# Optimization experiments

Measured on AMD Instinct MI355X. Metric: run time of the kernel, lower is better.

Reference implementation:

```python
import jax, jax.numpy as jnp
import numpy as np

HIDDEN = 2048
N_HEADS = 16
N_KV_HEADS = 4
HEAD_DIM = HIDDEN // N_HEADS  # 128
WINDOW = 2048
ROPE_THETA = 10000.0


def setup_inputs() -> dict:
    key = jax.random.key(0)
    ks = jax.random.split(key, 5)
    B, S = 1, 4096
    scale = 0.02
    return {
        "hidden_states": jax.random.normal(ks[0], (B, S, HIDDEN), dtype=jnp.float32),
        # nn.Linear weights are [out_features, in_features]
        "q_w": jax.random.normal(ks[1], (N_HEADS * HEAD_DIM, HIDDEN), dtype=jnp.float32) * scale,
        "k_w": jax.random.normal(ks[2], (N_KV_HEADS * HEAD_DIM, HIDDEN), dtype=jnp.float32) * scale,
        "v_w": jax.random.normal(ks[3], (N_KV_HEADS * HEAD_DIM, HIDDEN), dtype=jnp.float32) * scale,
        "o_w": jax.random.normal(ks[4], (HIDDEN, N_HEADS * HEAD_DIM), dtype=jnp.float32) * scale,
    }


def _rope_cos_sin(seq_len, dtype):
    inv_freq = 1.0 / (ROPE_THETA ** (jnp.arange(0, HEAD_DIM, 2, dtype=jnp.float32) / HEAD_DIM))
    pos = jnp.arange(seq_len, dtype=jnp.float32)
    freqs = pos[:, None] * inv_freq[None, :]          # [S, D/2]
    emb = jnp.concatenate([freqs, freqs], axis=-1)    # [S, D]
    return jnp.cos(emb).astype(dtype), jnp.sin(emb).astype(dtype)


def _rotate_half(x):
    x1, x2 = jnp.split(x, 2, axis=-1)
    return jnp.concatenate([-x2, x1], axis=-1)


def reference(hidden_states, q_w, k_w, v_w, o_w):
    B, S, _ = hidden_states.shape
    dtype = hidden_states.dtype

    q = hidden_states @ q_w.T                         # [B,S,H*D]
    k = hidden_states @ k_w.T                         # [B,S,Hkv*D]
    v = hidden_states @ v_w.T

    q = q.reshape(B, S, N_HEADS, HEAD_DIM).transpose(0, 2, 1, 3)      # [B,H,S,D]
    k = k.reshape(B, S, N_KV_HEADS, HEAD_DIM).transpose(0, 2, 1, 3)   # [B,Hkv,S,D]
    v = v.reshape(B, S, N_KV_HEADS, HEAD_DIM).transpose(0, 2, 1, 3)

    cos, sin = _rope_cos_sin(S, dtype)                # [S,D]
    cos = cos[None, None]
    sin = sin[None, None]
    q = q * cos + _rotate_half(q) * sin
    k = k * cos + _rotate_half(k) * sin

    n_rep = N_HEADS // N_KV_HEADS
    k = jnp.repeat(k, n_rep, axis=1)                  # [B,H,S,D]
    v = jnp.repeat(v, n_rep, axis=1)

    scores = jnp.einsum("bhqd,bhkd->bhqk", q, k) / jnp.sqrt(jnp.array(HEAD_DIM, dtype))

    pos = jnp.arange(S)
    rel = pos[:, None] - pos[None, :]
    allowed = (rel >= 0) & (rel < WINDOW)             # causal sliding window
    mask = jnp.where(allowed, jnp.array(0.0, dtype), jnp.array(-jnp.inf, dtype))
    scores = scores + mask[None, None]

    attn = jax.nn.softmax(scores.astype(jnp.float32), axis=-1).astype(dtype)

    out = jnp.einsum("bhqk,bhkd->bhqd", attn, v)      # [B,H,S,D]
    out = out.transpose(0, 2, 1, 3).reshape(B, S, N_HEADS * HEAD_DIM)
    return out @ o_w.T
```

## Files before the change

kernel.cpp:

```cpp
#include <hip/hip_runtime.h>
#include <stdint.h>

typedef unsigned short u16;
typedef unsigned int u32;
typedef float f32x4 __attribute__((ext_vector_type(4)));
typedef float f32x8 __attribute__((ext_vector_type(8)));
typedef int   i32x4 __attribute__((ext_vector_type(4)));
typedef __bf16 bf16x8 __attribute__((ext_vector_type(8)));
typedef u16 u16x4 __attribute__((ext_vector_type(4)));

constexpr int S_LEN = 4096;
constexpr int HID   = 2048;
constexpr int WIN   = 2048;

__device__ __forceinline__ u32 f2bf_u(float f) {
  u32 u = __builtin_bit_cast(u32, f);
  return (u + 0x7fffu + ((u >> 16) & 1u)) >> 16;
}
__device__ __forceinline__ float bf2f(u16 u) {
  return __builtin_bit_cast(float, ((u32)u) << 16);
}
__device__ __forceinline__ float exp2x(float x) {
#if __has_builtin(__builtin_amdgcn_exp2f)
  return __builtin_amdgcn_exp2f(x);
#else
  return exp2f(x);
#endif
}
__device__ __forceinline__ void mfma16(f32x4& acc, i32x4 a, i32x4 b) {
  acc = __builtin_amdgcn_mfma_f32_16x16x32_bf16(
      __builtin_bit_cast(bf16x8, a), __builtin_bit_cast(bf16x8, b), acc, 0, 0, 0);
}
__device__ __forceinline__ void gload_lds16(const u16* g, u16* l) {
  __builtin_amdgcn_global_load_lds((const __attribute__((address_space(1))) u32*)g,
                                   (__attribute__((address_space(3))) u32*)l, 16, 0, 0);
}

constexpr int CVT_B0 = 1048576;
constexpr int CVT_B1 = CVT_B0 + 524288;
constexpr int CVT_B2 = CVT_B1 + 131072;
constexpr int CVT_B3 = CVT_B2 + 131072;
constexpr int CVT_B4 = CVT_B3 + 524288;

__global__ __launch_bounds__(256) void cvt_all_kernel(
    const float* __restrict__ s0, const float* __restrict__ s1,
    const float* __restrict__ s2, const float* __restrict__ s3,
    const float* __restrict__ s4, u16* __restrict__ d0, u16* __restrict__ d1,
    u16* __restrict__ d2, u16* __restrict__ d3, u16* __restrict__ d4) {
  int t = blockIdx.x * 256 + threadIdx.x;
  const float* s;
  u16* d;
  int off;
  if (t < CVT_B0) { s = s0; d = d0; off = t; }
  else if (t < CVT_B1) { s = s1; d = d1; off = t - CVT_B0; }
  else if (t < CVT_B2) { s = s2; d = d2; off = t - CVT_B1; }
  else if (t < CVT_B3) { s = s3; d = d3; off = t - CVT_B2; }
  else { s = s4; d = d4; off = t - CVT_B3; }
  const f32x4* sp = (const f32x4*)s + (size_t)off * 2;
  f32x4 a = sp[0], b = sp[1];
  i32x4 o;
  o.x = (int)(f2bf_u(a.x) | (f2bf_u(a.y) << 16));
  o.y = (int)(f2bf_u(a.z) | (f2bf_u(a.w) << 16));
  o.z = (int)(f2bf_u(b.x) | (f2bf_u(b.y) << 16));
  o.w = (int)(f2bf_u(b.z) | (f2bf_u(b.w) << 16));
  *((i32x4*)d + off) = o;
}

__global__ __launch_bounds__(256) void rope_table_kernel(float* __restrict__ cs,
                                                         float* __restrict__ sn) {
  int t = blockIdx.x * 256 + threadIdx.x;
  int d = t & 63, s = t >> 6;
  float inv = exp2f(-(float)d * 0.20762050593046014f);
  float f = (float)s * inv;
  cs[t] = cosf(f);
  sn[t] = sinf(f);
}

__global__ __launch_bounds__(256) void rope_qk_kernel(u16* __restrict__ Qb,
                                                      u16* __restrict__ Kb,
                                                      const float* __restrict__ cs,
                                                      const float* __restrict__ sn) {
  const float SC2 = 0.088388347648318447f * 1.4426950408889634f;
  int t = blockIdx.x * 256 + threadIdx.x;
  int d0 = (t & 15) * 4;
  int r = t >> 4;
  u16* p;
  int s;
  float qs;
  if (r < S_LEN * 16) {
    int h = r & 15; s = r >> 4;
    p = Qb + (size_t)s * HID + h * 128 + d0;
    qs = SC2;
  } else {
    int r2 = r - S_LEN * 16;
    int h = r2 & 3; s = r2 >> 2;
    p = Kb + (size_t)s * 512 + h * 128 + d0;
    qs = 1.f;
  }
  f32x4 c = *(const f32x4*)&cs[(s << 6) | d0];
  f32x4 si = *(const f32x4*)&sn[(s << 6) | d0];
  u16x4 a = *(u16x4*)p, b = *(u16x4*)(p + 64);
  u16x4 oa, ob;
#pragma unroll
  for (int j = 0; j < 4; ++j) {
    float x1 = bf2f(a[j]), x2 = bf2f(b[j]);
    oa[j] = (u16)f2bf_u((x1 * c[j] - x2 * si[j]) * qs);
    ob[j] = (u16)f2bf_u((x2 * c[j] + x1 * si[j]) * qs);
  }
  *(u16x4*)p = oa;
  *(u16x4*)(p + 64) = ob;
}

__global__ __launch_bounds__(256) void qkv_gemm_kernel(
    const u16* __restrict__ A, const u16* __restrict__ Wq,
    const u16* __restrict__ Wk, const u16* __restrict__ Wv,
    u16* __restrict__ Qb, u16* __restrict__ Kb, u16* __restrict__ Vt) {
  __shared__ __attribute__((aligned(16))) u16 sA[128 * 64];
  __shared__ __attribute__((aligned(16))) u16 sB[128 * 64];
  const int lane = threadIdx.x & 63;
  const int w = threadIdx.x >> 6;
  const int g = lane >> 4, ln = lane & 15;
  const int K = HID;

  int wgid = blockIdx.x;
  wgid = (wgid & 7) * 96 + (wgid >> 3);
  const int brow = (wgid / 24) * 128;
  const int bcol = (wgid % 24) * 128;

  const u16* B;
  u16* out;
  int bc, mode, N;
  if (bcol < 2048)      { B = Wq; out = Qb; bc = bcol;        N = 2048; mode = 0; }
  else if (bcol < 2560) { B = Wk; out = Kb; bc = bcol - 2048; N = 512;  mode = 0; }
  else                  { B = Wv; out = Vt; bc = bcol - 2560; N = 512;  mode = 1; }

  const int wr = (w >> 1) * 64, wc = (w & 1) * 64;
  f32x4 acc[4][4] = {};

  const int sr = w * 32 + (lane >> 3);
  const int scol = (lane & 7) * 8;
  const u16* Abase = A + (size_t)(brow + sr) * K + scol;
  const u16* Bbase = B + (size_t)(bc + sr) * K + scol;
  u16* sAdst = &sA[w * 2048];
  u16* sBdst = &sB[w * 2048];

  for (int k0 = 0; k0 < K; k0 += 64) {
    __syncthreads();
#pragma unroll
    for (int i = 0; i < 4; ++i) {
      gload_lds16(Abase + (size_t)i * 8 * K + k0, sAdst + i * 512);
      gload_lds16(Bbase + (size_t)i * 8 * K + k0, sBdst + i * 512);
    }
    __syncthreads();
#pragma unroll
    for (int kk = 0; kk < 2; ++kk) {
      i32x4 af[4], bfr[4];
#pragma unroll
      for (int m = 0; m < 4; ++m)
        af[m] = *(const i32x4*)&sA[(wr + m * 16 + ln) * 64 + kk * 32 + g * 8];
#pragma unroll
      for (int n = 0; n < 4; ++n)
        bfr[n] = *(const i32x4*)&sB[(wc + n * 16 + ln) * 64 + kk * 32 + g * 8];
#pragma unroll
      for (int m = 0; m < 4; ++m)
#pragma unroll
        for (int n = 0; n < 4; ++n) mfma16(acc[m][n], af[m], bfr[n]);
    }
  }

  const int orow0 = brow + wr + g * 4;
  const int ocol0 = bc + wc + ln;
#pragma unroll
  for (int m = 0; m < 4; ++m)
#pragma unroll
    for (int n = 0; n < 4; ++n)
#pragma unroll
      for (int j = 0; j < 4; ++j) {
        int row = orow0 + m * 16 + j;
        int col = ocol0 + n * 16;
        float v = acc[m][n][j];
        if (mode == 0) {
          out[(size_t)row * N + col] = (u16)f2bf_u(v);
        } else {
          int d = col & 127, kvh = col >> 7;
          int T = row >> 5, ks = row & 31;
          int tt = ks >> 4, gg = (ks >> 2) & 3, e = (tt << 2) | (ks & 3);
          size_t idx = (size_t)kvh * S_LEN * 128 + (size_t)T * 4096 +
                       (size_t)d * 32 + ((size_t)(gg ^ ((d >> 1) & 3)) << 3) + e;
          out[idx] = (u16)f2bf_u(v);
        }
      }
}

__global__ __launch_bounds__(256) void gemm_o_kernel(const u16* __restrict__ A,
                                                     const u16* __restrict__ B,
                                                     float* __restrict__ Cv,
                                                     int K, int N) {
  __shared__ __attribute__((aligned(16))) u16 sA[128 * 64];
  __shared__ __attribute__((aligned(16))) u16 sB[128 * 64];
  const int lane = threadIdx.x & 63;
  const int w = threadIdx.x >> 6;
  const int g = lane >> 4, ln = lane & 15;

  int wgid = blockIdx.y * gridDim.x + blockIdx.x;
  const int nwg = gridDim.x * gridDim.y;
  wgid = (wgid & 7) * (nwg >> 3) + (wgid >> 3);
  const int brow = (wgid / gridDim.x) * 128;
  const int bcol = (wgid % gridDim.x) * 128;
  const int wr = (w >> 1) * 64, wc = (w & 1) * 64;

  f32x4 acc[4][4] = {};

  const int sr = w * 32 + (lane >> 3);
  const int scol = (lane & 7) * 8;
  const u16* Abase = A + (size_t)(brow + sr) * K + scol;
  const u16* Bbase = B + (size_t)(bcol + sr) * K + scol;
  u16* sAdst = &sA[w * 2048];
  u16* sBdst = &sB[w * 2048];

  for (int k0 = 0; k0 < K; k0 += 64) {
    __syncthreads();
#pragma unroll
    for (int i = 0; i < 4; ++i) {
      gload_lds16(Abase + (size_t)i * 8 * K + k0, sAdst + i * 512);
      gload_lds16(Bbase + (size_t)i * 8 * K + k0, sBdst + i * 512);
    }
    __syncthreads();
#pragma unroll
    for (int kk = 0; kk < 2; ++kk) {
      i32x4 af[4], bfr[4];
#pragma unroll
      for (int m = 0; m < 4; ++m)
        af[m] = *(const i32x4*)&sA[(wr + m * 16 + ln) * 64 + kk * 32 + g * 8];
#pragma unroll
      for (int n = 0; n < 4; ++n)
        bfr[n] = *(const i32x4*)&sB[(wc + n * 16 + ln) * 64 + kk * 32 + g * 8];
#pragma unroll
      for (int m = 0; m < 4; ++m)
#pragma unroll
        for (int n = 0; n < 4; ++n) mfma16(acc[m][n], af[m], bfr[n]);
    }
  }

  const int orow0 = brow + wr + g * 4;
  const int ocol0 = bcol + wc + ln;
#pragma unroll
  for (int m = 0; m < 4; ++m)
#pragma unroll
    for (int n = 0; n < 4; ++n)
#pragma unroll
      for (int j = 0; j < 4; ++j)
        Cv[(size_t)(orow0 + m * 16 + j) * N + ocol0 + n * 16] = acc[m][n][j];
}

__global__ __launch_bounds__(64) void attn_kernel(const u16* __restrict__ Q,
                                                  const u16* __restrict__ Kb,
                                                  const u16* __restrict__ Vt,
                                                  u16* __restrict__ opart,
                                                  float* __restrict__ mpart,
                                                  float* __restrict__ lpart) {
  const int lane = threadIdx.x;
  const int g = lane >> 4, ln = lane & 15;

  const int o = blockIdx.x;
  const int wgid = ((o & 7) << 9) | (o >> 3);
  const int h = wgid >> 8;
  const int idx = wgid & 255;
  const int chunk = idx & 1;
  const int gq = 127 - (idx >> 1);
  const int kvh = h >> 2;
  const int qr0 = gq * 32;

  i32x4 aq[2][4];
#pragma unroll
  for (int qf = 0; qf < 2; ++qf) {
    const u16* qp = Q + (size_t)(qr0 + qf * 16 + ln) * HID + h * 128 + g * 8;
#pragma unroll
    for (int c = 0; c < 4; ++c) aq[qf][c] = *(const i32x4*)(qp + c * 32);
  }

  f32x4 oacc[2][8] = {};
  float mrun[2] = {-1e30f, -1e30f};
  float lrun[2] = {0.f, 0.f};

  int lo = qr0 - (WIN - 1);
  if (lo < 0) lo = 0;
  lo &= ~31;
  const int nt_full = ((qr0 + 32) - lo) >> 5;
  const int nt0 = nt_full >> 1;
  const int lo_c = lo + (chunk ? nt0 * 32 : 0);
  const int nt = chunk ? nt_full - nt0 : nt0;

  const u16* kptr = Kb + (size_t)(lo_c + ln) * 512 + kvh * 128 + g * 8;
  const int vswz = (g ^ ((ln >> 1) & 3)) << 3;
  const u16* vptr = Vt + (size_t)kvh * S_LEN * 128 +
                    (size_t)(lo_c >> 5) * 4096 + ln * 32 + vswz;

  i32x4 kf[2][4], vf[8];
  if (nt > 0) {
#pragma unroll
    for (int t = 0; t < 2; ++t)
#pragma unroll
      for (int c = 0; c < 4; ++c)
        kf[t][c] = *(const i32x4*)(kptr + t * 8192 + c * 32);
#pragma unroll
    for (int nf = 0; nf < 8; ++nf) vf[nf] = *(const i32x4*)(vptr + nf * 512);
  }

  for (int it = 0; it < nt; ++it) {
    const int kb = lo_c + it * 32;
    const bool more = (it + 1 < nt);

    f32x4 sc[2][2] = {};
    __builtin_amdgcn_s_setprio(1);
#pragma unroll
    for (int c = 0; c < 4; ++c) {
      mfma16(sc[0][0], kf[0][c], aq[0][c]);
      mfma16(sc[0][1], kf[1][c], aq[0][c]);
      mfma16(sc[1][0], kf[0][c], aq[1][c]);
      mfma16(sc[1][1], kf[1][c], aq[1][c]);
    }
    __builtin_amdgcn_s_setprio(0);

    if (more) {
      kptr += 32 * 512;
#pragma unroll
      for (int t = 0; t < 2; ++t)
#pragma unroll
        for (int c = 0; c < 4; ++c)
          kf[t][c] = *(const i32x4*)(kptr + t * 8192 + c * 32);
    }

    float p[2][8];
    float mx[2];
    const bool interior = (kb + 31 <= qr0) && (qr0 + 31 - kb < WIN);
#pragma unroll
    for (int qf = 0; qf < 2; ++qf) {
      if (interior) {
#pragma unroll
        for (int j = 0; j < 4; ++j) {
          p[qf][j] = sc[qf][0][j];
          p[qf][4 + j] = sc[qf][1][j];
        }
      } else {
        const float NEG = -__builtin_inff();
        const int q = qr0 + qf * 16 + ln;
#pragma unroll
        for (int t = 0; t < 2; ++t)
#pragma unroll
          for (int j = 0; j < 4; ++j) {
            int k = kb + t * 16 + g * 4 + j;
            p[qf][t * 4 + j] = (k <= q && q - k < WIN) ? sc[qf][t][j] : NEG;
          }
      }
      float x0 = fmaxf(fmaxf(p[qf][0], p[qf][1]), p[qf][2]);
      float x1 = fmaxf(fmaxf(p[qf][3], p[qf][4]), p[qf][5]);
      float x2 = fmaxf(fmaxf(p[qf][6], p[qf][7]), x0);
      float m = fmaxf(x1, x2);
      m = fmaxf(m, __shfl_xor(m, 16));
      m = fmaxf(m, __shfl_xor(m, 32));
      mx[qf] = m;
    }

    float corr[2] = {1.f, 1.f};
    const bool noskip =
        !__all((mx[0] - mrun[0] <= 11.f) && (mx[1] - mrun[1] <= 11.f));
    if (noskip) {
#pragma unroll
      for (int qf = 0; qf < 2; ++qf) {
        float mnew = fmaxf(mrun[qf], mx[qf]);
        corr[qf] = exp2x(mrun[qf] - mnew);
        mrun[qf] = mnew;
        f32x4 cv;
#pragma unroll
        for (int j = 0; j < 4; ++j) cv[j] = __shfl(corr[qf], g * 4 + j);
#pragma unroll
        for (int nf = 0; nf < 8; ++nf)
#pragma unroll
          for (int j = 0; j < 4; ++j) oacc[qf][nf][j] *= cv[j];
      }
    }

    i32x4 pa[2];
#pragma unroll
    for (int qf = 0; qf < 2; ++qf) {
      f32x8 pv;
#pragma unroll
      for (int e = 0; e < 8; ++e) pv[e] = exp2x(p[qf][e] - mrun[qf]);
      float rs = ((pv[0] + pv[1]) + (pv[2] + pv[3])) +
                 ((pv[4] + pv[5]) + (pv[6] + pv[7]));
      lrun[qf] = lrun[qf] * corr[qf] + rs;
      bf16x8 pb = __builtin_convertvector(pv, bf16x8);
      pa[qf] = __builtin_bit_cast(i32x4, pb);
    }

    __builtin_amdgcn_s_setprio(1);
#pragma unroll
    for (int nf = 0; nf < 8; ++nf) {
      mfma16(oacc[0][nf], pa[0], vf[nf]);
      mfma16(oacc[1][nf], pa[1], vf[nf]);
    }
    __builtin_amdgcn_s_setprio(0);

    if (more) {
      vptr += 4096;
#pragma unroll
      for (int nf = 0; nf < 8; ++nf) vf[nf] = *(const i32x4*)(vptr + nf * 512);
    }
  }

#pragma unroll
  for (int qf = 0; qf < 2; ++qf) {
    float l = lrun[qf];
    l += __shfl_xor(l, 16);
    l += __shfl_xor(l, 32);
    lrun[qf] = l;
  }

  const size_t pb = ((size_t)chunk * 16 + h) * S_LEN;
#pragma unroll
  for (int qf = 0; qf < 2; ++qf) {
    if (g == 0) {
      mpart[pb + qr0 + qf * 16 + ln] = mrun[qf];
      lpart[pb + qr0 + qf * 16 + ln] = lrun[qf];
    }
    u16* aop = opart + (pb + qr0 + qf * 16 + g * 4) * 128 + ln;
#pragma unroll
    for (int j = 0; j < 4; ++j)
#pragma unroll
      for (int nf = 0; nf < 8; ++nf)
        aop[(size_t)j * 128 + nf * 16] = (u16)f2bf_u(oacc[qf][nf][j]);
  }
}

__global__ __launch_bounds__(256) void attn_combine_kernel(
    const u16* __restrict__ opart, const float* __restrict__ mpart,
    const float* __restrict__ lpart, u16* __restrict__ AO) {
  int t = blockIdx.x * 256 + threadIdx.x;
  int d0 = (t & 15) * 8;
  int rh = t >> 4;
  int row = rh & (S_LEN - 1);
  int h = rh >> 12;
  size_t i0 = (size_t)h * S_LEN + row;
  size_t i1 = i0 + (size_t)16 * S_LEN;
  float m0 = mpart[i0], m1 = mpart[i1];
  float l0 = lpart[i0], l1 = lpart[i1];
  float m = fmaxf(m0, m1);
  float w0 = exp2x(m0 - m), w1 = exp2x(m1 - m);
  float inv = 1.f / (l0 * w0 + l1 * w1);
  w0 *= inv;
  w1 *= inv;
  i32x4 v0 = *(const i32x4*)(opart + i0 * 128 + d0);
  i32x4 v1 = *(const i32x4*)(opart + i1 * 128 + d0);
  i32x4 ov;
#pragma unroll
  for (int j = 0; j < 4; ++j) {
    u32 a = ((u32)v0[j]), b = ((u32)v1[j]);
    float x = bf2f((u16)a) * w0 + bf2f((u16)b) * w1;
    float y = bf2f((u16)(a >> 16)) * w0 + bf2f((u16)(b >> 16)) * w1;
    ov[j] = (int)(f2bf_u(x) | (f2bf_u(y) << 16));
  }
  *(i32x4*)(AO + (size_t)row * HID + h * 128 + d0) = ov;
}

extern "C" void kernel_launch(void* const* d_in, const int* in_sizes, int n_in,
                              void* d_out, int out_size, void* d_ws, size_t ws_size,
                              hipStream_t stream) {
  const float* hx = (const float*)d_in[0];
  const float* qw = (const float*)d_in[1];
  const float* kw = (const float*)d_in[2];
  const float* vw = (const float*)d_in[3];
  const float* ow = (const float*)d_in[4];

  char* p = (char*)d_ws;
  u16* Xb = (u16*)p; p += (size_t)S_LEN * HID * 2;
  u16* Wq = (u16*)p; p += (size_t)HID * HID * 2;
  u16* Wk = (u16*)p; p += (size_t)512 * HID * 2;
  u16* Wv = (u16*)p; p += (size_t)512 * HID * 2;
  u16* Wo = (u16*)p; p += (size_t)HID * HID * 2;
  u16* Qb = (u16*)p; p += (size_t)S_LEN * HID * 2;
  u16* Kb = (u16*)p; p += (size_t)S_LEN * 512 * 2;
  u16* Vt = (u16*)p; p += (size_t)S_LEN * 512 * 2;
  u16* AO = (u16*)p; p += (size_t)S_LEN * HID * 2;
  float* cs = (float*)p; p += (size_t)S_LEN * 64 * 4;
  float* sn = (float*)p; p += (size_t)S_LEN * 64 * 4;
  u16* Opart = (u16*)p; p += (size_t)2 * 16 * S_LEN * 128 * 2;
  float* Mpart = (float*)p; p += (size_t)2 * 16 * S_LEN * 4;
  float* Lpart = (float*)p; p += (size_t)2 * 16 * S_LEN * 4;

  cvt_all_kernel<<<CVT_B4 / 256, 256, 0, stream>>>(hx, qw, kw, vw, ow, Xb, Wq,
                                                   Wk, Wv, Wo);
  rope_table_kernel<<<S_LEN * 64 / 256, 256, 0, stream>>>(cs, sn);

  qkv_gemm_kernel<<<768, 256, 0, stream>>>(Xb, Wq, Wk, Wv, Qb, Kb, Vt);

  rope_qk_kernel<<<S_LEN * 20 * 16 / 256, 256, 0, stream>>>(Qb, Kb, cs, sn);

  attn_kernel<<<4096, 64, 0, stream>>>(Qb, Kb, Vt, Opart, Mpart, Lpart);
  attn_combine_kernel<<<S_LEN * 16 * 16 / 256, 256, 0, stream>>>(Opart, Mpart,
                                                                 Lpart, AO);

  gemm_o_kernel<<<dim3(16, 32), 256, 0, stream>>>(AO, Wo, (float*)d_out, HID,
                                                  HID);
}
```

Measured before the change: 315.6 us.

## Double-buffer swizzled 256x128 GEMM core for QKV and O projections; fold rope table into convert

Replaces the two single-buffered 128x128 GEMMs with a shared 256x128-tile core run by 512-thread blocks. The core double-buffers LDS via global_load_lds with vmcnt waits and XOR-swizzles the LDS layout to cut bank conflicts. It also folds rope table generation into the conversion kernel, removing one launch. This raises LDS use to 96KB per block, which limits occupancy, and reduces grid sizes to 384 and 256 blocks.

Result: faster. 298.0 us (median of 3 runs) (-5.6%).

```diff
diff --git a/kernel.cpp b/kernel.cpp
--- a/kernel.cpp
+++ b/kernel.cpp
@@ -41,13 +41,28 @@
 constexpr int CVT_B2 = CVT_B1 + 131072;
 constexpr int CVT_B3 = CVT_B2 + 131072;
 constexpr int CVT_B4 = CVT_B3 + 524288;
+constexpr int CVT_B5 = CVT_B4 + 32768;
 
 __global__ __launch_bounds__(256) void cvt_all_kernel(
     const float* __restrict__ s0, const float* __restrict__ s1,
     const float* __restrict__ s2, const float* __restrict__ s3,
     const float* __restrict__ s4, u16* __restrict__ d0, u16* __restrict__ d1,
-    u16* __restrict__ d2, u16* __restrict__ d3, u16* __restrict__ d4) {
+    u16* __restrict__ d2, u16* __restrict__ d3, u16* __restrict__ d4,
+    float* __restrict__ cs, float* __restrict__ sn) {
   int t = blockIdx.x * 256 + threadIdx.x;
+  if (t >= CVT_B4) {
+    if (t >= CVT_B5) return;
+    int e = (t - CVT_B4) * 8;
+    int d = e & 63, s = e >> 6;
+#pragma unroll
+    for (int j = 0; j < 8; ++j) {
+      float inv = exp2f(-(float)(d + j) * 0.20762050593046014f);
+      float f = (float)s * inv;
+      cs[e + j] = cosf(f);
+      sn[e + j] = sinf(f);
+    }
+    return;
+  }
   const float* s;
   u16* d;
   int off;
@@ -64,16 +79,6 @@
   o.z = (int)(f2bf_u(b.x) | (f2bf_u(b.y) << 16));
   o.w = (int)(f2bf_u(b.z) | (f2bf_u(b.w) << 16));
   *((i32x4*)d + off) = o;
-}
-
-__global__ __launch_bounds__(256) void rope_table_kernel(float* __restrict__ cs,
-                                                         float* __restrict__ sn) {
-  int t = blockIdx.x * 256 + threadIdx.x;
-  int d = t & 63, s = t >> 6;
-  float inv = exp2f(-(float)d * 0.20762050593046014f);
-  float f = (float)s * inv;
-  cs[t] = cosf(f);
-  sn[t] = sinf(f);
 }
 
 __global__ __launch_bounds__(256) void rope_qk_kernel(u16* __restrict__ Qb,
@@ -111,65 +116,96 @@
   *(u16x4*)(p + 64) = ob;
 }
 
-__global__ __launch_bounds__(256) void qkv_gemm_kernel(
+__device__ __forceinline__ void gemm256_core(const u16* __restrict__ A_,
+                                             const u16* __restrict__ Bm_,
+                                             int brow_, int bc_,
+                                             f32x4 (&acc)[4][4], int& orow0,
+                                             int& ocol0) {
+  __shared__ __attribute__((aligned(16))) u16 sA[2][256 * 64];
+  __shared__ __attribute__((aligned(16))) u16 sB[2][128 * 64];
+  const int t = threadIdx.x;
+  const int lane = t & 63;
+  const int w = t >> 6;
+  const int g = lane >> 4, ln = lane & 15;
+  const int wm = w >> 1, wn = w & 1;
+  const int trow = t >> 3, tslot = t & 7;
+  const int sslot = tslot ^ (trow & 7);
+  const u16* Abase = A_ + (size_t)(brow_ + trow) * 2048 + sslot * 8;
+  const u16* Bbase = Bm_ + (size_t)(bc_ + trow) * 2048 + sslot * 8;
+
+#define STAGE6(buf, kt)                                                        \
+  {                                                                            \
+    const int _k0 = (kt) * 64;                                                 \
+    _Pragma("unroll") for (int a2 = 0; a2 < 4; ++a2)                           \
+        gload_lds16(Abase + (size_t)a2 * 64 * 2048 + _k0,                      \
+                    &sA[buf][a2 * 4096 + t * 8]);                              \
+    _Pragma("unroll") for (int b2 = 0; b2 < 2; ++b2)                           \
+        gload_lds16(Bbase + (size_t)b2 * 64 * 2048 + _k0,                      \
+                    &sB[buf][b2 * 4096 + t * 8]);                              \
+  }
+
+  STAGE6(0, 0);
+  STAGE6(1, 1);
+  asm volatile("s_waitcnt vmcnt(6)" ::: "memory");
+  __builtin_amdgcn_s_barrier();
+  int cur = 0;
+  for (int kt = 0; kt < 32; ++kt) {
+    i32x4 bfr[4][2];
+#pragma unroll
+    for (int n = 0; n < 4; ++n) {
+      const int row = wn * 64 + n * 16 + ln;
+      const int sw = row & 7;
+      bfr[n][0] = *(const i32x4*)&sB[cur][row * 64 + ((g ^ sw) << 3)];
+      bfr[n][1] = *(const i32x4*)&sB[cur][row * 64 + (((4 | g) ^ sw) << 3)];
+    }
+    __builtin_amdgcn_s_setprio(1);
+#pragma unroll
+    for (int m = 0; m < 4; ++m) {
+      const int row = wm * 64 + m * 16 + ln;
+      const int sw = row & 7;
+      i32x4 a0 = *(const i32x4*)&sA[cur][row * 64 + ((g ^ sw) << 3)];
+      i32x4 a1 = *(const i32x4*)&sA[cur][row * 64 + (((4 | g) ^ sw) << 3)];
+#pragma unroll
+      for (int n = 0; n < 4; ++n) {
+        mfma16(acc[m][n], a0, bfr[n][0]);
+        mfma16(acc[m][n], a1, bfr[n][1]);
+      }
+    }
+    __builtin_amdgcn_s_setprio(0);
+    __builtin_amdgcn_s_barrier();
+    if (kt + 2 < 32) {
+      STAGE6(cur, kt + 2);
+      asm volatile("s_waitcnt vmcnt(6)" ::: "memory");
+    } else if (kt + 1 < 32) {
+      asm volatile("s_waitcnt vmcnt(0)" ::: "memory");
+    }
+    __builtin_amdgcn_s_barrier();
+    cur ^= 1;
+  }
+#undef STAGE6
+  orow0 = brow_ + wm * 64 + g * 4;
+  ocol0 = bc_ + wn * 64 + ln;
+}
+
+__global__ __launch_bounds__(512) void qkv256_kernel(
     const u16* __restrict__ A, const u16* __restrict__ Wq,
     const u16* __restrict__ Wk, const u16* __restrict__ Wv,
     u16* __restrict__ Qb, u16* __restrict__ Kb, u16* __restrict__ Vt) {
-  __shared__ __attribute__((aligned(16))) u16 sA[128 * 64];
-  __shared__ __attribute__((aligned(16))) u16 sB[128 * 64];
-  const int lane = threadIdx.x & 63;
-  const int w = threadIdx.x >> 6;
-  const int g = lane >> 4, ln = lane & 15;
-  const int K = HID;
-
   int wgid = blockIdx.x;
-  wgid = (wgid & 7) * 96 + (wgid >> 3);
-  const int brow = (wgid / 24) * 128;
+  wgid = (wgid & 7) * 48 + (wgid >> 3);
+  const int brow = (wgid / 24) * 256;
   const int bcol = (wgid % 24) * 128;
-
-  const u16* B;
+  const u16* Bm;
   u16* out;
   int bc, mode, N;
-  if (bcol < 2048)      { B = Wq; out = Qb; bc = bcol;        N = 2048; mode = 0; }
-  else if (bcol < 2560) { B = Wk; out = Kb; bc = bcol - 2048; N = 512;  mode = 0; }
-  else                  { B = Wv; out = Vt; bc = bcol - 2560; N = 512;  mode = 1; }
-
-  const int wr = (w >> 1) * 64, wc = (w & 1) * 64;
+  if (bcol < 2048)      { Bm = Wq; out = Qb; bc = bcol;        N = 2048; mode = 0; }
+  else if (bcol < 2560) { Bm = Wk; out = Kb; bc = bcol - 2048; N = 512;  mode = 0; }
+  else                  { Bm = Wv; out = Vt; bc = bcol - 2560; N = 512;  mode = 1; }
+
   f32x4 acc[4][4] = {};
-
-  const int sr = w * 32 + (lane >> 3);
-  const int scol = (lane & 7) * 8;
-  const u16* Abase = A + (size_t)(brow + sr) * K + scol;
-  const u16* Bbase = B + (size_t)(bc + sr) * K + scol;
-  u16* sAdst = &sA[w * 2048];
-  u16* sBdst = &sB[w * 2048];
-
-  for (int k0 = 0; k0 < K; k0 += 64) {
-    __syncthreads();
-#pragma unroll
-    for (int i = 0; i < 4; ++i) {
-      gload_lds16(Abase + (size_t)i * 8 * K + k0, sAdst + i * 512);
-      gload_lds16(Bbase + (size_t)i * 8 * K + k0, sBdst + i * 512);
-    }
-    __syncthreads();
-#pragma unroll
-    for (int kk = 0; kk < 2; ++kk) {
-      i32x4 af[4], bfr[4];
-#pragma unroll
-      for (int m = 0; m < 4; ++m)
-        af[m] = *(const i32x4*)&sA[(wr + m * 16 + ln) * 64 + kk * 32 + g * 8];
-#pragma unroll
-      for (int n = 0; n < 4; ++n)
-        bfr[n] = *(const i32x4*)&sB[(wc + n * 16 + ln) * 64 + kk * 32 + g * 8];
-#pragma unroll
-      for (int m = 0; m < 4; ++m)
-#pragma unroll
-        for (int n = 0; n < 4; ++n) mfma16(acc[m][n], af[m], bfr[n]);
-    }
-  }
-
-  const int orow0 = brow + wr + g * 4;
-  const int ocol0 = bc + wc + ln;
+  int orow0, ocol0;
+  gemm256_core(A, Bm, brow, bc, acc, orow0, ocol0);
+
 #pragma unroll
   for (int m = 0; m < 4; ++m)
 #pragma unroll
@@ -192,65 +228,25 @@
       }
 }
 
-__global__ __launch_bounds__(256) void gemm_o_kernel(const u16* __restrict__ A,
-                                                     const u16* __restrict__ B,
-                                                     float* __restrict__ Cv,
-                                                     int K, int N) {
-  __shared__ __attribute__((aligned(16))) u16 sA[128 * 64];
-  __shared__ __attribute__((aligned(16))) u16 sB[128 * 64];
-  const int lane = threadIdx.x & 63;
-  const int w = threadIdx.x >> 6;
-  const int g = lane >> 4, ln = lane & 15;
-
-  int wgid = blockIdx.y * gridDim.x + blockIdx.x;
-  const int nwg = gridDim.x * gridDim.y;
-  wgid = (wgid & 7) * (nwg >> 3) + (wgid >> 3);
-  const int brow = (wgid / gridDim.x) * 128;
-  const int bcol = (wgid % gridDim.x) * 128;
-  const int wr = (w >> 1) * 64, wc = (w & 1) * 64;
+__global__ __launch_bounds__(512) void o256_kernel(const u16* __restrict__ A,
+                                                   const u16* __restrict__ Bw,
+                                                   float* __restrict__ Cv) {
+  int wgid = blockIdx.x;
+  wgid = (wgid & 7) * 32 + (wgid >> 3);
+  const int brow = (wgid / 16) * 256;
+  const int bcol = (wgid % 16) * 128;
 
   f32x4 acc[4][4] = {};
-
-  const int sr = w * 32 + (lane >> 3);
-  const int scol = (lane & 7) * 8;
-  const u16* Abase = A + (size_t)(brow + sr) * K + scol;
-  const u16* Bbase = B + (size_t)(bcol + sr) * K + scol;
-  u16* sAdst = &sA[w * 2048];
-  u16* sBdst = &sB[w * 2048];
-
-  for (int k0 = 0; k0 < K; k0 += 64) {
-    __syncthreads();
-#pragma unroll
-    for (int i = 0; i < 4; ++i) {
-      gload_lds16(Abase + (size_t)i * 8 * K + k0, sAdst + i * 512);
-      gload_lds16(Bbase + (size_t)i * 8 * K + k0, sBdst + i * 512);
-    }
-    __syncthreads();
-#pragma unroll
-    for (int kk = 0; kk < 2; ++kk) {
-      i32x4 af[4], bfr[4];
-#pragma unroll
-      for (int m = 0; m < 4; ++m)
-        af[m] = *(const i32x4*)&sA[(wr + m * 16 + ln) * 64 + kk * 32 + g * 8];
-#pragma unroll
-      for (int n = 0; n < 4; ++n)
-        bfr[n] = *(const i32x4*)&sB[(wc + n * 16 + ln) * 64 + kk * 32 + g * 8];
-#pragma unroll
-      for (int m = 0; m < 4; ++m)
-#pragma unroll
-        for (int n = 0; n < 4; ++n) mfma16(acc[m][n], af[m], bfr[n]);
-    }
-  }
-
-  const int orow0 = brow + wr + g * 4;
-  const int ocol0 = bcol + wc + ln;
+  int orow0, ocol0;
+  gemm256_core(A, Bw, brow, bcol, acc, orow0, ocol0);
+
 #pragma unroll
   for (int m = 0; m < 4; ++m)
 #pragma unroll
     for (int n = 0; n < 4; ++n)
 #pragma unroll
       for (int j = 0; j < 4; ++j)
-        Cv[(size_t)(orow0 + m * 16 + j) * N + ocol0 + n * 16] = acc[m][n][j];
+        Cv[(size_t)(orow0 + m * 16 + j) * 2048 + ocol0 + n * 16] = acc[m][n][j];
 }
 
 __global__ __launch_bounds__(64) void attn_kernel(const u16* __restrict__ Q,
@@ -299,10 +295,10 @@
   i32x4 kf[2][4], vf[8];
   if (nt > 0) {
 #pragma unroll
-    for (int t = 0; t < 2; ++t)
+    for (int tt = 0; tt < 2; ++tt)
 #pragma unroll
       for (int c = 0; c < 4; ++c)
-        kf[t][c] = *(const i32x4*)(kptr + t * 8192 + c * 32);
+        kf[tt][c] = *(const i32x4*)(kptr + tt * 8192 + c * 32);
 #pragma unroll
     for (int nf = 0; nf < 8; ++nf) vf[nf] = *(const i32x4*)(vptr + nf * 512);
   }
@@ -325,10 +321,10 @@
     if (more) {
       kptr += 32 * 512;
 #pragma unroll
-      for (int t = 0; t < 2; ++t)
+      for (int tt = 0; tt < 2; ++tt)
 #pragma unroll
         for (int c = 0; c < 4; ++c)
-          kf[t][c] = *(const i32x4*)(kptr + t * 8192 + c * 32);
+          kf[tt][c] = *(const i32x4*)(kptr + tt * 8192 + c * 32);
     }
 
     float p[2][8];
@@ -346,11 +342,11 @@
         const float NEG = -__builtin_inff();
         const int q = qr0 + qf * 16 + ln;
 #pragma unroll
-        for (int t = 0; t < 2; ++t)
+        for (int tt = 0; tt < 2; ++tt)
 #pragma unroll
           for (int j = 0; j < 4; ++j) {
-            int k = kb + t * 16 + g * 4 + j;
-            p[qf][t * 4 + j] = (k <= q && q - k < WIN) ? sc[qf][t][j] : NEG;
+            int k = kb + tt * 16 + g * 4 + j;
+            p[qf][tt * 4 + j] = (k <= q && q - k < WIN) ? sc[qf][tt][j] : NEG;
           }
       }
       float x0 = fmaxf(fmaxf(p[qf][0], p[qf][1]), p[qf][2]);
@@ -488,11 +484,10 @@
   float* Mpart = (float*)p; p += (size_t)2 * 16 * S_LEN * 4;
   float* Lpart = (float*)p; p += (size_t)2 * 16 * S_LEN * 4;
 
-  cvt_all_kernel<<<CVT_B4 / 256, 256, 0, stream>>>(hx, qw, kw, vw, ow, Xb, Wq,
-                                                   Wk, Wv, Wo);
-  rope_table_kernel<<<S_LEN * 64 / 256, 256, 0, stream>>>(cs, sn);
-
-  qkv_gemm_kernel<<<768, 256, 0, stream>>>(Xb, Wq, Wk, Wv, Qb, Kb, Vt);
+  cvt_all_kernel<<<(CVT_B5 + 255) / 256, 256, 0, stream>>>(
+      hx, qw, kw, vw, ow, Xb, Wq, Wk, Wv, Wo, cs, sn);
+
+  qkv256_kernel<<<384, 512, 0, stream>>>(Xb, Wq, Wk, Wv, Qb, Kb, Vt);
 
   rope_qk_kernel<<<S_LEN * 20 * 16 / 256, 256, 0, stream>>>(Qb, Kb, cs, sn);
 
@@ -500,6 +495,5 @@
   attn_combine_kernel<<<S_LEN * 16 * 16 / 256, 256, 0, stream>>>(Opart, Mpart,
                                                                  Lpart, AO);
 
-  gemm_o_kernel<<<dim3(16, 32), 256, 0, stream>>>(AO, Wo, (float*)d_out, HID,
-                                                  HID);
-}
+  o256_kernel<<<256, 512, 0, stream>>>(AO, Wo, (float*)d_out);
+}
```
